# Kernel tuning notes

Measured on AMD Instinct MI355X. Metric: run time of the kernel, lower is better.

Reference implementation:

```python
import jax, jax.numpy as jnp
import numpy as np

NEG_SLOPE = 0.2


def gcn_conv(x, W, b, src, dst, w, n):
    # x: [N, F_in], W: [F_in, F_out], edge (src -> dst) with weight w.
    xw = x @ W  # [N, F_out]
    # add self-loops with weight 1 (PyG GCNConv default)
    loop = jnp.arange(n)
    src_f = jnp.concatenate([src, loop])
    dst_f = jnp.concatenate([dst, loop])
    w_f = jnp.concatenate([w, jnp.ones((n,), dtype=w.dtype)])
    # symmetric normalization: deg computed on destination
    deg = jax.ops.segment_sum(w_f, dst_f, num_segments=n)
    dinv = jnp.where(deg > 0, jax.lax.rsqrt(deg), 0.0)
    norm = dinv[src_f] * w_f * dinv[dst_f]  # [E+N]
    msg = xw[src_f] * norm[:, None]          # [E+N, F_out]
    out = jax.ops.segment_sum(msg, dst_f, num_segments=n)
    return out + b


def setup_inputs() -> dict:
    key = jax.random.key(0)
    k1, k2, k3, k4, k5 = jax.random.split(key, 5)
    N, E, F_in, F_hid, F_out = 100000, 3200000, 128, 128, 64
    x = jax.random.normal(k1, (N, F_in), dtype=jnp.float32)
    edge_index = jax.random.randint(k2, (2, E), 0, N, dtype=jnp.int64)
    edge_weight = jax.random.uniform(k3, (E,), dtype=jnp.float32)
    s1 = 1.0 / np.sqrt(F_in)
    s2 = 1.0 / np.sqrt(F_hid)
    W1 = jax.random.uniform(k4, (F_in, F_hid), minval=-s1, maxval=s1, dtype=jnp.float32)
    b1 = jnp.zeros((F_hid,), dtype=jnp.float32)
    W2 = jax.random.uniform(k5, (F_hid, F_out), minval=-s2, maxval=s2, dtype=jnp.float32)
    b2 = jnp.zeros((F_out,), dtype=jnp.float32)
    return {"x": x, "edge_index": edge_index, "edge_weight": edge_weight,
            "W1": W1, "b1": b1, "W2": W2, "b2": b2}


def reference(x, edge_index, edge_weight, W1, b1, W2, b2):
    n = x.shape[0]
    src, dst = edge_index[0], edge_index[1]
    h = gcn_conv(x, W1, b1, src, dst, edge_weight, n)
    h = jax.nn.leaky_relu(h, NEG_SLOPE)
    # dropout is identity in eval mode
    h = gcn_conv(h, W2, b2, src, dst, edge_weight, n)
    return jax.nn.log_softmax(h, axis=1)
```

## Files before the change

### kernel.cpp

```cpp
#include <hip/hip_runtime.h>
#include <cstdint>
#include <cstddef>

#define NEG_SLOPE 0.2f
#define CH 8192
#define CAP 6144
#define BN 128

typedef short v8s __attribute__((ext_vector_type(8)));
typedef float v4f __attribute__((ext_vector_type(4)));

static __device__ __forceinline__ float b2f(unsigned short u) {
  return __uint_as_float((unsigned)u << 16);
}
static __device__ __forceinline__ unsigned short f2b(float f) {
  unsigned u = __float_as_uint(f);
  return (unsigned short)((u + 0x7FFFu + ((u >> 16) & 1u)) >> 16);
}
static __device__ __forceinline__ ushort4 f2b4(float4 v) {
  ushort4 r; r.x = f2b(v.x); r.y = f2b(v.y); r.z = f2b(v.z); r.w = f2b(v.w); return r;
}
static __device__ __forceinline__ int pk(float lo, float hi) {
  return (int)((unsigned)f2b(lo) | ((unsigned)f2b(hi) << 16));
}

static __device__ __forceinline__ int edge_at(const void* ei, int is32, long long pos) {
  return is32 ? ((const int*)ei)[pos] : (int)(((const long long*)ei)[pos]);
}

__global__ void k_init(unsigned* gcur, int nb) {
  int i = blockIdx.x * blockDim.x + threadIdx.x;
  if (i < nb) gcur[i] = 0u;
}

__global__ __launch_bounds__(256) void k_partgemm(const void* __restrict__ ei, const float* __restrict__ ew,
                                                  int2* __restrict__ recs, unsigned* __restrict__ gcur,
                                                  int E, int nb, int nchunks,
                                                  const float* __restrict__ X, const float* __restrict__ W,
                                                  unsigned short* __restrict__ Y, int M) {
  __shared__ int4 sm4[2560];
  __shared__ int is32sh;
  int tid = threadIdx.x;

  if (blockIdx.x < nchunks) {
    unsigned* hist  = (unsigned*)sm4;
    unsigned* bas   = (unsigned*)sm4 + 1024;
    unsigned* erank = (unsigned*)sm4 + 2048;
    if (tid == 0) is32sh = 0;
    for (int i = tid; i < nb; i += 256) hist[i] = 0u;
    __syncthreads();
    if (((const int*)ei)[2 * tid + 1] != 0) atomicOr(&is32sh, 1);
    __syncthreads();
    int is32 = is32sh;
    int c0 = blockIdx.x * CH;
#pragma unroll
    for (int j = 0; j < CH / 256; ++j) {
      int idx = c0 + j * 256 + tid;
      if (idx < E) {
        int d = edge_at(ei, is32, (long long)E + idx);
        int b = d >> 7, dl = d & (BN - 1);
        unsigned r = atomicAdd(&hist[b], 1u);
        erank[j * 256 + tid] = ((unsigned)b << 20) | ((unsigned)dl << 13) | r;
      }
    }
    __syncthreads();
    for (int i = tid; i < nb; i += 256) {
      unsigned c = hist[i];
      bas[i] = c ? atomicAdd(&gcur[i], c) : 0u;
    }
    __syncthreads();
#pragma unroll
    for (int j = 0; j < CH / 256; ++j) {
      int idx = c0 + j * 256 + tid;
      if (idx < E) {
        unsigned er = erank[j * 256 + tid];
        int b = (int)(er >> 20);
        int dl = (int)((er >> 13) & (BN - 1));
        unsigned p = bas[b] + (er & 8191u);
        if (p < CAP) {
          int s = edge_at(ei, is32, idx);
          float w = ew[idx];
          recs[(size_t)b * CAP + p] = make_int2(s | (dl << 17), __float_as_int(w));
        }
      }
    }
  } else {
    int4* XsV = sm4;
    int wv = tid >> 6, ln = tid & 63;
    int row0 = (blockIdx.x - nchunks) * 128;
    int lq = ln >> 4, lr = ln & 15;

    v8s bfr[4][2];
#pragma unroll
    for (int kst = 0; kst < 4; ++kst)
#pragma unroll
      for (int ni = 0; ni < 2; ++ni) {
        int col = wv * 32 + ni * 16 + lr;
#pragma unroll
        for (int j = 0; j < 8; ++j) {
          int k = kst * 32 + lq * 8 + j;
          bfr[kst][ni][j] = (short)f2b(W[k * 128 + col]);
        }
      }

#pragma unroll
    for (int j = 0; j < 8; ++j) {
      int idx = j * 256 + tid;
      int row = idx >> 4, u = idx & 15;
      int gr = row0 + row;
      int4 out = make_int4(0, 0, 0, 0);
      if (gr < M) {
        float4 a  = ((const float4*)X)[(size_t)gr * 32 + u * 2];
        float4 bq = ((const float4*)X)[(size_t)gr * 32 + u * 2 + 1];
        out = make_int4(pk(a.x, a.y), pk(a.z, a.w), pk(bq.x, bq.y), pk(bq.z, bq.w));
      }
      XsV[row * 16 + (u ^ (row & 7))] = out;
    }
    __syncthreads();

    v4f acc[8][2];
#pragma unroll
    for (int mi = 0; mi < 8; ++mi)
#pragma unroll
      for (int ni = 0; ni < 2; ++ni) acc[mi][ni] = (v4f)(0.0f);

#pragma unroll
    for (int kst = 0; kst < 4; ++kst) {
      int u = kst * 4 + lq;
#pragma unroll
      for (int mi = 0; mi < 8; ++mi) {
        int row = mi * 16 + lr;
        v8s a = *(const v8s*)&XsV[row * 16 + (u ^ (row & 7))];
#pragma unroll
        for (int ni = 0; ni < 2; ++ni)
          acc[mi][ni] = __builtin_amdgcn_mfma_f32_16x16x32_bf16(a, bfr[kst][ni], acc[mi][ni], 0, 0, 0);
      }
    }

#pragma unroll
    for (int mi = 0; mi < 8; ++mi) {
#pragma unroll
      for (int ni = 0; ni < 2; ++ni) {
        int col = wv * 32 + ni * 16 + lr;
#pragma unroll
        for (int r = 0; r < 4; ++r) {
          int grow = row0 + mi * 16 + lq * 4 + r;
          if (grow < M) Y[(size_t)grow * 128 + col] = f2b(acc[mi][ni][r]);
        }
      }
    }
  }
}

__global__ __launch_bounds__(256) void k_deg(const int2* __restrict__ recs, const unsigned* __restrict__ gcur,
                                             float* __restrict__ dinv, int2* __restrict__ rp2, int N) {
  __shared__ float degL[BN];
  __shared__ unsigned cntL[BN], pref[BN];
  int b = blockIdx.x, tid = threadIdx.x;
  if (tid < BN) { degL[tid] = 1.0f; cntL[tid] = 0u; }
  __syncthreads();
  int cnt = min((int)gcur[b], CAP);
  const int2* rb = recs + (size_t)b * CAP;
  for (int e = tid; e < cnt; e += 256) {
    int2 rc = rb[e];
    int dl = (rc.x >> 17) & (BN - 1);
    atomicAdd(&degL[dl], __int_as_float(rc.y));
    atomicAdd(&cntL[dl], 1u);
  }
  __syncthreads();
  if (tid < BN) pref[tid] = cntL[tid];
  __syncthreads();
  for (int d = 1; d < BN; d <<= 1) {
    unsigned v = 0u;
    if (tid < BN && tid >= d) v = pref[tid - d];
    __syncthreads();
    if (tid < BN) pref[tid] += v;
    __syncthreads();
  }
  int gnode = b * BN + tid;
  if (tid < BN && gnode < N) {
    dinv[gnode] = rsqrtf(degL[tid]);
    unsigned st = pref[tid] - cntL[tid];
    rp2[gnode] = make_int2(b * CAP + (int)st, b * CAP + (int)pref[tid]);
  }
}

__global__ __launch_bounds__(256) void k_bin(const int2* __restrict__ recs, const unsigned* __restrict__ gcur,
                                             const float* __restrict__ dinv, const int2* __restrict__ rp2,
                                             int2* __restrict__ pairs, int N) {
  __shared__ unsigned baseL[BN], cnt2[BN];
  int b = blockIdx.x, tid = threadIdx.x;
  if (tid < BN) {
    int gnode = b * BN + tid;
    baseL[tid] = (gnode < N) ? (unsigned)(rp2[gnode].x - b * CAP) : 0u;
    cnt2[tid] = 0u;
  }
  __syncthreads();
  int cnt = min((int)gcur[b], CAP);
  const int2* rb = recs + (size_t)b * CAP;
  for (int e = tid; e < cnt; e += 256) {
    int2 rc = rb[e];
    int dl = (rc.x >> 17) & (BN - 1);
    int s = rc.x & 0x1FFFF;
    unsigned r = atomicAdd(&cnt2[dl], 1u);
    float nm = dinv[s] * __int_as_float(rc.y);
    pairs[(size_t)b * CAP + baseL[dl] + r] = make_int2(s, __float_as_int(nm));
  }
}

template <int FOUT>
__global__ __launch_bounds__(256) void k_gemmM(const void* __restrict__ Xv,
                                               const float* __restrict__ W,
                                               unsigned short* __restrict__ Y, int M) {
  constexpr int NI = FOUT / 64;
  __shared__ int4 XsV[128 * 16];
  int t = threadIdx.x;
  int wv = t >> 6, ln = t & 63;
  int row0 = blockIdx.x * 128;
  int lq = ln >> 4, lr = ln & 15;

  v8s bfr[4][NI];
#pragma unroll
  for (int kst = 0; kst < 4; ++kst)
#pragma unroll
    for (int ni = 0; ni < NI; ++ni) {
      int col = wv * (16 * NI) + ni * 16 + lr;
#pragma unroll
      for (int j = 0; j < 8; ++j) {
        int k = kst * 32 + lq * 8 + j;
        bfr[kst][ni][j] = (short)f2b(W[k * FOUT + col]);
      }
    }

#pragma unroll
  for (int j = 0; j < 8; ++j) {
    int idx = j * 256 + t;
    int row = idx >> 4, u = idx & 15;
    int gr = row0 + row;
    int4 out = make_int4(0, 0, 0, 0);
    if (gr < M) out = ((const int4*)Xv)[(size_t)gr * 16 + u];
    XsV[row * 16 + (u ^ (row & 7))] = out;
  }
  __syncthreads();

  v4f acc[8][NI];
#pragma unroll
  for (int mi = 0; mi < 8; ++mi)
#pragma unroll
    for (int ni = 0; ni < NI; ++ni) acc[mi][ni] = (v4f)(0.0f);

#pragma unroll
  for (int kst = 0; kst < 4; ++kst) {
    int u = kst * 4 + lq;
#pragma unroll
    for (int mi = 0; mi < 8; ++mi) {
      int row = mi * 16 + lr;
      v8s a = *(const v8s*)&XsV[row * 16 + (u ^ (row & 7))];
#pragma unroll
      for (int ni = 0; ni < NI; ++ni)
        acc[mi][ni] = __builtin_amdgcn_mfma_f32_16x16x32_bf16(a, bfr[kst][ni], acc[mi][ni], 0, 0, 0);
    }
  }

#pragma unroll
  for (int mi = 0; mi < 8; ++mi) {
#pragma unroll
    for (int ni = 0; ni < NI; ++ni) {
      int col = wv * (16 * NI) + ni * 16 + lr;
#pragma unroll
      for (int r = 0; r < 4; ++r) {
        int grow = row0 + mi * 16 + lq * 4 + r;
        if (grow < M) Y[(size_t)grow * FOUT + col] = f2b(acc[mi][ni][r]);
      }
    }
  }
}

__global__ __launch_bounds__(256) void k_agg1(const ushort4* __restrict__ xwb, const float* __restrict__ dinv,
                                              const int2* __restrict__ rp2, const int2* __restrict__ pairs,
                                              const float* __restrict__ b1,
                                              ushort4* __restrict__ hb, int n) {
  int wid = threadIdx.x >> 6;
  int lane = threadIdx.x & 63;
  int node = blockIdx.x * 4 + wid;
  if (node >= n) return;
  int half = lane >> 5;
  int fo = lane & 31;
  float di = dinv[node];
  float4 acc = make_float4(0.f, 0.f, 0.f, 0.f);
  int2 rr = rp2[node];
  int e = rr.x, e1 = rr.y;
  for (; e + 16 <= e1; e += 16) {
    int2 p[8];
#pragma unroll
    for (int j = 0; j < 8; ++j) p[j] = pairs[e + 2 * j + half];
    ushort4 v[8];
#pragma unroll
    for (int j = 0; j < 8; ++j) v[j] = xwb[(size_t)p[j].x * 32 + fo];
#pragma unroll
    for (int j = 0; j < 8; ++j) {
      float nm = __int_as_float(p[j].y);
      acc.x = fmaf(b2f(v[j].x), nm, acc.x);
      acc.y = fmaf(b2f(v[j].y), nm, acc.y);
      acc.z = fmaf(b2f(v[j].z), nm, acc.z);
      acc.w = fmaf(b2f(v[j].w), nm, acc.w);
    }
  }
  for (; e < e1; e += 2) {
    int ee = e + half;
    if (ee < e1) {
      int2 p = pairs[ee];
      ushort4 v = xwb[(size_t)p.x * 32 + fo];
      float nm = __int_as_float(p.y);
      acc.x = fmaf(b2f(v.x), nm, acc.x);
      acc.y = fmaf(b2f(v.y), nm, acc.y);
      acc.z = fmaf(b2f(v.z), nm, acc.z);
      acc.w = fmaf(b2f(v.w), nm, acc.w);
    }
  }
  acc.x += __shfl_xor(acc.x, 32, 64);
  acc.y += __shfl_xor(acc.y, 32, 64);
  acc.z += __shfl_xor(acc.z, 32, 64);
  acc.w += __shfl_xor(acc.w, 32, 64);
  ushort4 sv = xwb[(size_t)node * 32 + fo];
  acc.x = fmaf(b2f(sv.x), di, acc.x);
  acc.y = fmaf(b2f(sv.y), di, acc.y);
  acc.z = fmaf(b2f(sv.z), di, acc.z);
  acc.w = fmaf(b2f(sv.w), di, acc.w);
  float4 b = ((const float4*)b1)[fo];
  acc.x = fmaf(acc.x, di, b.x);
  acc.y = fmaf(acc.y, di, b.y);
  acc.z = fmaf(acc.z, di, b.z);
  acc.w = fmaf(acc.w, di, b.w);
  acc.x = acc.x > 0.f ? acc.x : NEG_SLOPE * acc.x;
  acc.y = acc.y > 0.f ? acc.y : NEG_SLOPE * acc.y;
  acc.z = acc.z > 0.f ? acc.z : NEG_SLOPE * acc.z;
  acc.w = acc.w > 0.f ? acc.w : NEG_SLOPE * acc.w;
  if (half == 0) hb[(size_t)node * 32 + fo] = f2b4(acc);
}

__global__ __launch_bounds__(256) void k_agg2(const ushort4* __restrict__ hwb, const float* __restrict__ dinv,
                                              const int2* __restrict__ rp2, const int2* __restrict__ pairs,
                                              const float* __restrict__ b2,
                                              float* __restrict__ out, int n) {
  int wid = threadIdx.x >> 6;
  int lane = threadIdx.x & 63;
  int node = blockIdx.x * 4 + wid;
  if (node >= n) return;
  int q = lane >> 4;
  int fo = lane & 15;
  float di = dinv[node];
  float4 acc = make_float4(0.f, 0.f, 0.f, 0.f);
  int2 rr = rp2[node];
  int e = rr.x, e1 = rr.y;
  for (; e + 32 <= e1; e += 32) {
    int2 p[8];
#pragma unroll
    for (int j = 0; j < 8; ++j) p[j] = pairs[e + 4 * j + q];
    ushort4 v[8];
#pragma unroll
    for (int j = 0; j < 8; ++j) v[j] = hwb[(size_t)p[j].x * 16 + fo];
#pragma unroll
    for (int j = 0; j < 8; ++j) {
      float nm = __int_as_float(p[j].y);
      acc.x = fmaf(b2f(v[j].x), nm, acc.x);
      acc.y = fmaf(b2f(v[j].y), nm, acc.y);
      acc.z = fmaf(b2f(v[j].z), nm, acc.z);
      acc.w = fmaf(b2f(v[j].w), nm, acc.w);
    }
  }
  for (; e < e1; e += 4) {
    int ee = e + q;
    if (ee < e1) {
      int2 p = pairs[ee];
      ushort4 v = hwb[(size_t)p.x * 16 + fo];
      float nm = __int_as_float(p.y);
      acc.x = fmaf(b2f(v.x), nm, acc.x);
      acc.y = fmaf(b2f(v.y), nm, acc.y);
      acc.z = fmaf(b2f(v.z), nm, acc.z);
      acc.w = fmaf(b2f(v.w), nm, acc.w);
    }
  }
#pragma unroll
  for (int d = 32; d >= 16; d >>= 1) {
    acc.x += __shfl_xor(acc.x, d, 64);
    acc.y += __shfl_xor(acc.y, d, 64);
    acc.z += __shfl_xor(acc.z, d, 64);
    acc.w += __shfl_xor(acc.w, d, 64);
  }
  ushort4 sv = hwb[(size_t)node * 16 + fo];
  acc.x = fmaf(b2f(sv.x), di, acc.x);
  acc.y = fmaf(b2f(sv.y), di, acc.y);
  acc.z = fmaf(b2f(sv.z), di, acc.z);
  acc.w = fmaf(b2f(sv.w), di, acc.w);
  float4 b = ((const float4*)b2)[fo];
  acc.x = fmaf(acc.x, di, b.x);
  acc.y = fmaf(acc.y, di, b.y);
  acc.z = fmaf(acc.z, di, b.z);
  acc.w = fmaf(acc.w, di, b.w);
  float m = fmaxf(fmaxf(acc.x, acc.y), fmaxf(acc.z, acc.w));
#pragma unroll
  for (int d = 8; d >= 1; d >>= 1) m = fmaxf(m, __shfl_xor(m, d, 64));
  float s = expf(acc.x - m) + expf(acc.y - m) + expf(acc.z - m) + expf(acc.w - m);
#pragma unroll
  for (int d = 8; d >= 1; d >>= 1) s += __shfl_xor(s, d, 64);
  float lse = m + logf(s);
  if (q == 0) {
    float4 o = make_float4(acc.x - lse, acc.y - lse, acc.z - lse, acc.w - lse);
    ((float4*)out)[(size_t)node * 16 + fo] = o;
  }
}

extern "C" void kernel_launch(void* const* d_in, const int* in_sizes, int n_in,
                              void* d_out, int out_size, void* d_ws, size_t ws_size,
                              hipStream_t stream) {
  const float* x  = (const float*)d_in[0];
  const void*  ei = d_in[1];
  const float* ew = (const float*)d_in[2];
  const float* W1 = (const float*)d_in[3];
  const float* b1 = (const float*)d_in[4];
  const float* W2 = (const float*)d_in[5];
  const float* b2 = (const float*)d_in[6];
  float* out = (float*)d_out;

  const int Fh = in_sizes[4];
  const int Fi = in_sizes[3] / Fh;
  const int N  = in_sizes[0] / Fi;
  const int E  = in_sizes[2];
  const int NB = (N + BN - 1) / BN;

  char* ws = (char*)d_ws;
  size_t o = 0;
  auto alloc = [&](size_t bytes) { size_t r = o; o += (bytes + 255) & ~(size_t)255; return r; };
  ushort4* xwb  = (ushort4*)(ws + alloc((size_t)N * 128 * 2));
  ushort4* hb   = (ushort4*)(ws + alloc((size_t)N * 128 * 2));
  int2*    prs  = (int2*)   (ws + alloc((size_t)NB * CAP * 8));
  int2*    recs = (int2*)   (ws + alloc((size_t)NB * CAP * 8));
  float*   dinv = (float*)  (ws + alloc((size_t)N * 4));
  int2*    rp2  = (int2*)   (ws + alloc((size_t)(N + BN) * 8));
  unsigned* gcur= (unsigned*)(ws + alloc((size_t)NB * 4));
  (void)ws_size;

  const int tb = 256;
  const int nchunks = (E + CH - 1) / CH;
  const int ngemm1 = (N + 127) / 128;

  hipLaunchKernelGGL(k_init,     dim3((NB + tb - 1) / tb), dim3(tb), 0, stream, gcur, NB);
  hipLaunchKernelGGL(k_partgemm, dim3(nchunks + ngemm1), dim3(tb), 0, stream,
                     ei, ew, recs, gcur, E, NB, nchunks,
                     x, W1, (unsigned short*)xwb, N);
  hipLaunchKernelGGL(k_deg,      dim3(NB), dim3(tb), 0, stream, recs, gcur, dinv, rp2, N);
  hipLaunchKernelGGL(k_bin,      dim3(NB), dim3(tb), 0, stream, recs, gcur, dinv, rp2, prs, N);

  hipLaunchKernelGGL(k_agg1,     dim3((N + 3) / 4), dim3(tb), 0, stream, xwb, dinv, rp2, prs, b1, hb, N);
  hipLaunchKernelGGL((k_gemmM<64>), dim3((N + 127) / 128), dim3(tb), 0, stream,
                     (const void*)hb, W2, (unsigned short*)xwb, N);
  hipLaunchKernelGGL(k_agg2,     dim3((N + 3) / 4), dim3(tb), 0, stream, xwb, dinv, rp2, prs, b2, out, N);
}
```

Measured before the change: 346.9 us.

## Fuse degree and binning kernels, shrink partition LDS, defer dinv[src] to aggregation

The separate degree and binning kernels become one k_build kernel, so the bucket records are read once more inside the same block instead of in a second launch. The source-side dinv factor is no longer baked into the pairs. Both aggregation kernels now gather dinv[src] per edge, which adds a random 4-byte load per edge in each layer. The partition kernel stores only 16-bit ranks in LDS and re-reads the destination index, and the fused GEMM tile is halved to 64 rows to cut LDS use and raise occupancy.

```diff
diff --git a/kernel.cpp b/kernel.cpp
--- a/kernel.cpp
+++ b/kernel.cpp
@@ -38,14 +38,14 @@
                                                   int E, int nb, int nchunks,
                                                   const float* __restrict__ X, const float* __restrict__ W,
                                                   unsigned short* __restrict__ Y, int M) {
-  __shared__ int4 sm4[2560];
+  __shared__ int4 sm4[1536];
   __shared__ int is32sh;
   int tid = threadIdx.x;
 
   if (blockIdx.x < nchunks) {
-    unsigned* hist  = (unsigned*)sm4;
-    unsigned* bas   = (unsigned*)sm4 + 1024;
-    unsigned* erank = (unsigned*)sm4 + 2048;
+    unsigned* hist = (unsigned*)sm4;
+    unsigned* bas  = (unsigned*)sm4 + 800;
+    unsigned short* erank = (unsigned short*)((unsigned*)sm4 + 1600);
     if (tid == 0) is32sh = 0;
     for (int i = tid; i < nb; i += 256) hist[i] = 0u;
     __syncthreads();
@@ -53,30 +53,28 @@
     __syncthreads();
     int is32 = is32sh;
     int c0 = blockIdx.x * CH;
+#pragma unroll
+    for (int j = 0; j < CH / 256; ++j) {
+      int idx = c0 + j * 256 + tid;
+      if (idx < E) {
+        int d = edge_at(ei, is32, (long long)E + idx);
+        unsigned r = atomicAdd(&hist[d >> 7], 1u);
+        erank[j * 256 + tid] = (unsigned short)r;
+      }
+    }
+    __syncthreads();
+    for (int i = tid; i < nb; i += 256) {
+      unsigned c = hist[i];
+      bas[i] = c ? atomicAdd(&gcur[i], c) : 0u;
+    }
+    __syncthreads();
 #pragma unroll
     for (int j = 0; j < CH / 256; ++j) {
       int idx = c0 + j * 256 + tid;
       if (idx < E) {
         int d = edge_at(ei, is32, (long long)E + idx);
         int b = d >> 7, dl = d & (BN - 1);
-        unsigned r = atomicAdd(&hist[b], 1u);
-        erank[j * 256 + tid] = ((unsigned)b << 20) | ((unsigned)dl << 13) | r;
-      }
-    }
-    __syncthreads();
-    for (int i = tid; i < nb; i += 256) {
-      unsigned c = hist[i];
-      bas[i] = c ? atomicAdd(&gcur[i], c) : 0u;
-    }
-    __syncthreads();
-#pragma unroll
-    for (int j = 0; j < CH / 256; ++j) {
-      int idx = c0 + j * 256 + tid;
-      if (idx < E) {
-        unsigned er = erank[j * 256 + tid];
-        int b = (int)(er >> 20);
-        int dl = (int)((er >> 13) & (BN - 1));
-        unsigned p = bas[b] + (er & 8191u);
+        unsigned p = bas[b] + erank[j * 256 + tid];
         if (p < CAP) {
           int s = edge_at(ei, is32, idx);
           float w = ew[idx];
@@ -87,7 +85,7 @@
   } else {
     int4* XsV = sm4;
     int wv = tid >> 6, ln = tid & 63;
-    int row0 = (blockIdx.x - nchunks) * 128;
+    int row0 = (blockIdx.x - nchunks) * 64;
     int lq = ln >> 4, lr = ln & 15;
 
     v8s bfr[4][2];
@@ -104,7 +102,7 @@
       }
 
 #pragma unroll
-    for (int j = 0; j < 8; ++j) {
+    for (int j = 0; j < 4; ++j) {
       int idx = j * 256 + tid;
       int row = idx >> 4, u = idx & 15;
       int gr = row0 + row;
@@ -118,9 +116,9 @@
     }
     __syncthreads();
 
-    v4f acc[8][2];
-#pragma unroll
-    for (int mi = 0; mi < 8; ++mi)
+    v4f acc[4][2];
+#pragma unroll
+    for (int mi = 0; mi < 4; ++mi)
 #pragma unroll
       for (int ni = 0; ni < 2; ++ni) acc[mi][ni] = (v4f)(0.0f);
 
@@ -128,7 +126,7 @@
     for (int kst = 0; kst < 4; ++kst) {
       int u = kst * 4 + lq;
 #pragma unroll
-      for (int mi = 0; mi < 8; ++mi) {
+      for (int mi = 0; mi < 4; ++mi) {
         int row = mi * 16 + lr;
         v8s a = *(const v8s*)&XsV[row * 16 + (u ^ (row & 7))];
 #pragma unroll
@@ -138,7 +136,7 @@
     }
 
 #pragma unroll
-    for (int mi = 0; mi < 8; ++mi) {
+    for (int mi = 0; mi < 4; ++mi) {
 #pragma unroll
       for (int ni = 0; ni < 2; ++ni) {
         int col = wv * 32 + ni * 16 + lr;
@@ -152,12 +150,13 @@
   }
 }
 
-__global__ __launch_bounds__(256) void k_deg(const int2* __restrict__ recs, const unsigned* __restrict__ gcur,
-                                             float* __restrict__ dinv, int2* __restrict__ rp2, int N) {
+__global__ __launch_bounds__(256) void k_build(const int2* __restrict__ recs, const unsigned* __restrict__ gcur,
+                                               float* __restrict__ dinv, int2* __restrict__ rp2,
+                                               int2* __restrict__ pairs, int N) {
   __shared__ float degL[BN];
-  __shared__ unsigned cntL[BN], pref[BN];
+  __shared__ unsigned cntL[BN], pref[BN], cnt2[BN];
   int b = blockIdx.x, tid = threadIdx.x;
-  if (tid < BN) { degL[tid] = 1.0f; cntL[tid] = 0u; }
+  if (tid < BN) { degL[tid] = 1.0f; cntL[tid] = 0u; cnt2[tid] = 0u; }
   __syncthreads();
   int cnt = min((int)gcur[b], CAP);
   const int2* rb = recs + (size_t)b * CAP;
@@ -183,28 +182,13 @@
     unsigned st = pref[tid] - cntL[tid];
     rp2[gnode] = make_int2(b * CAP + (int)st, b * CAP + (int)pref[tid]);
   }
-}
-
-__global__ __launch_bounds__(256) void k_bin(const int2* __restrict__ recs, const unsigned* __restrict__ gcur,
-                                             const float* __restrict__ dinv, const int2* __restrict__ rp2,
-                                             int2* __restrict__ pairs, int N) {
-  __shared__ unsigned baseL[BN], cnt2[BN];
-  int b = blockIdx.x, tid = threadIdx.x;
-  if (tid < BN) {
-    int gnode = b * BN + tid;
-    baseL[tid] = (gnode < N) ? (unsigned)(rp2[gnode].x - b * CAP) : 0u;
-    cnt2[tid] = 0u;
-  }
   __syncthreads();
-  int cnt = min((int)gcur[b], CAP);
-  const int2* rb = recs + (size_t)b * CAP;
   for (int e = tid; e < cnt; e += 256) {
     int2 rc = rb[e];
     int dl = (rc.x >> 17) & (BN - 1);
-    int s = rc.x & 0x1FFFF;
     unsigned r = atomicAdd(&cnt2[dl], 1u);
-    float nm = dinv[s] * __int_as_float(rc.y);
-    pairs[(size_t)b * CAP + baseL[dl] + r] = make_int2(s, __float_as_int(nm));
+    unsigned pos = (pref[dl] - cntL[dl]) + r;
+    pairs[(size_t)b * CAP + pos] = make_int2(rc.x & 0x1FFFF, rc.y);
   }
 }
 
@@ -294,12 +278,15 @@
     int2 p[8];
 #pragma unroll
     for (int j = 0; j < 8; ++j) p[j] = pairs[e + 2 * j + half];
+    float ds[8];
+#pragma unroll
+    for (int j = 0; j < 8; ++j) ds[j] = dinv[p[j].x];
     ushort4 v[8];
 #pragma unroll
     for (int j = 0; j < 8; ++j) v[j] = xwb[(size_t)p[j].x * 32 + fo];
 #pragma unroll
     for (int j = 0; j < 8; ++j) {
-      float nm = __int_as_float(p[j].y);
+      float nm = ds[j] * __int_as_float(p[j].y);
       acc.x = fmaf(b2f(v[j].x), nm, acc.x);
       acc.y = fmaf(b2f(v[j].y), nm, acc.y);
       acc.z = fmaf(b2f(v[j].z), nm, acc.z);
@@ -311,7 +298,7 @@
     if (ee < e1) {
       int2 p = pairs[ee];
       ushort4 v = xwb[(size_t)p.x * 32 + fo];
-      float nm = __int_as_float(p.y);
+      float nm = dinv[p.x] * __int_as_float(p.y);
       acc.x = fmaf(b2f(v.x), nm, acc.x);
       acc.y = fmaf(b2f(v.y), nm, acc.y);
       acc.z = fmaf(b2f(v.z), nm, acc.z);
@@ -357,12 +344,15 @@
     int2 p[8];
 #pragma unroll
     for (int j = 0; j < 8; ++j) p[j] = pairs[e + 4 * j + q];
+    float ds[8];
+#pragma unroll
+    for (int j = 0; j < 8; ++j) ds[j] = dinv[p[j].x];
     ushort4 v[8];
 #pragma unroll
     for (int j = 0; j < 8; ++j) v[j] = hwb[(size_t)p[j].x * 16 + fo];
 #pragma unroll
     for (int j = 0; j < 8; ++j) {
-      float nm = __int_as_float(p[j].y);
+      float nm = ds[j] * __int_as_float(p[j].y);
       acc.x = fmaf(b2f(v[j].x), nm, acc.x);
       acc.y = fmaf(b2f(v[j].y), nm, acc.y);
       acc.z = fmaf(b2f(v[j].z), nm, acc.z);
@@ -374,7 +364,7 @@
     if (ee < e1) {
       int2 p = pairs[ee];
       ushort4 v = hwb[(size_t)p.x * 16 + fo];
-      float nm = __int_as_float(p.y);
+      float nm = dinv[p.x] * __int_as_float(p.y);
       acc.x = fmaf(b2f(v.x), nm, acc.x);
       acc.y = fmaf(b2f(v.y), nm, acc.y);
       acc.z = fmaf(b2f(v.z), nm, acc.z);
@@ -443,14 +433,13 @@
 
   const int tb = 256;
   const int nchunks = (E + CH - 1) / CH;
-  const int ngemm1 = (N + 127) / 128;
+  const int ngemm1 = (N + 63) / 64;
 
   hipLaunchKernelGGL(k_init,     dim3((NB + tb - 1) / tb), dim3(tb), 0, stream, gcur, NB);
   hipLaunchKernelGGL(k_partgemm, dim3(nchunks + ngemm1), dim3(tb), 0, stream,
                      ei, ew, recs, gcur, E, NB, nchunks,
                      x, W1, (unsigned short*)xwb, N);
-  hipLaunchKernelGGL(k_deg,      dim3(NB), dim3(tb), 0, stream, recs, gcur, dinv, rp2, N);
-  hipLaunchKernelGGL(k_bin,      dim3(NB), dim3(tb), 0, stream, recs, gcur, dinv, rp2, prs, N);
+  hipLaunchKernelGGL(k_build,    dim3(NB), dim3(tb), 0, stream, recs, gcur, dinv, rp2, prs, N);
 
   hipLaunchKernelGGL(k_agg1,     dim3((N + 3) / 4), dim3(tb), 0, stream, xwb, dinv, rp2, prs, b1, hb, N);
   hipLaunchKernelGGL((k_gemmM<64>), dim3((N + 127) / 128), dim3(tb), 0, stream,
```

Measured after the change: 349.6 us. No clear change (+0.8%).
